# Kernel optimization log

Hardware: AMD Instinct MI355X
Metric: run time of the kernel (lower is better)

Reference implementation:

```python
import jax, jax.numpy as jnp
import numpy as np

B, S, D, N = 8, 4096, 1024, 64
EPS = 1e-5


def setup_inputs() -> dict:
    key = jax.random.key(0)
    ks = jax.random.split(key, 6)
    sD = 1.0 / np.sqrt(D)
    sN = 1.0 / np.sqrt(N)
    return {
        "x": jax.random.normal(ks[0], (B, S, D), dtype=jnp.float32),
        "ln_w": jnp.ones((D,), jnp.float32),
        "ln_b": jnp.zeros((D,), jnp.float32),
        "Wi": jax.random.normal(ks[1], (N, D), jnp.float32) * sD,
        "bi": jnp.zeros((N,), jnp.float32),
        "Wf": jax.random.normal(ks[2], (N, D), jnp.float32) * sD,
        "bf": jnp.zeros((N,), jnp.float32),
        "Wz": jax.random.normal(ks[3], (N, D), jnp.float32) * sD,
        "bz": jnp.zeros((N,), jnp.float32),
        "Wo": jax.random.normal(ks[4], (N, D), jnp.float32) * sD,
        "bo": jnp.zeros((N,), jnp.float32),
        "Wp": jax.random.normal(ks[5], (D, N), jnp.float32) * sN,
        "bp": jnp.zeros((D,), jnp.float32),
    }


def reference(x, ln_w, ln_b, Wi, bi, Wf, bf, Wz, bz, Wo, bo, Wp, bp):
    # LayerNorm over last dim (eps matches torch default 1e-5)
    mu = jnp.mean(x, axis=-1, keepdims=True)
    var = jnp.mean(jnp.square(x - mu), axis=-1, keepdims=True)
    xn = (x - mu) * jax.lax.rsqrt(var + EPS) * ln_w + ln_b

    # Precompute all four projections as batched GEMMs: (B,S,N)
    log_i = jnp.clip(jnp.einsum('bsd,nd->bsn', xn, Wi) + bi, -20.0, 20.0)
    log_f = jnp.clip(jnp.einsum('bsd,nd->bsn', xn, Wf) + bf, -20.0, 20.0)
    z = jnp.tanh(jnp.einsum('bsd,nd->bsn', xn, Wz) + bz)
    o = jax.nn.sigmoid(jnp.einsum('bsd,nd->bsn', xn, Wo) + bo)

    # Stabilized exponential-gated recurrence via lax.scan over time
    def step(carry, inp):
        c, m = carry
        li, lf, zt, ot = inp
        m_new = jnp.maximum(m + lf, li)
        i_s = jnp.exp(li - m_new)
        f_s = jnp.exp(m + lf - m_new)
        c = f_s * c + i_s * zt
        h = ot * jnp.tanh(c)
        return (c, m_new), h

    c0 = jnp.zeros((x.shape[0], log_i.shape[-1]), x.dtype)
    m0 = jnp.zeros_like(c0)
    # time-major inputs: (S,B,N)
    tm = lambda a: jnp.swapaxes(a, 0, 1)
    _, h_seq = jax.lax.scan(step, (c0, m0), (tm(log_i), tm(log_f), tm(z), tm(o)))
    h_seq = jnp.swapaxes(h_seq, 0, 1)  # (B,S,N)

    return jnp.einsum('bsn,dn->bsd', h_seq, Wp) + bp
```

## Files before the change

kernel.cpp:

```cpp
#include <hip/hip_runtime.h>
#include <hip/hip_bf16.h>

#define BB 8
#define SS 4096
#define DD 1024
#define NN 64
#define ROWS (BB * SS)
#define GLD 256
#define NCHUNK 256
#define CLEN 16

typedef _Float16 f16;
using f16x8 = __attribute__((ext_vector_type(8))) _Float16;
using f32x4 = __attribute__((ext_vector_type(4))) float;

__global__ void prep_pack(const float* __restrict__ Wi, const float* __restrict__ Wf,
                          const float* __restrict__ Wz, const float* __restrict__ Wo,
                          const float* __restrict__ Wp, const float* __restrict__ ln_w,
                          f16* __restrict__ Wpk, f16* __restrict__ Wpf) {
    int i = blockIdx.x * 256 + threadIdx.x;
    if (i < 32768) {
        int l = i & 63, cb = (i >> 6) & 15, s = i >> 10;
        int r = cb * 16 + (l & 15);
        int c = s * 32 + (l >> 4) * 8;
        int g = r >> 6, rem = r & 63;
        const float* W = (g == 0) ? Wi : (g == 1) ? Wf : (g == 2) ? Wz : Wo;
        const float* src = W + rem * 1024 + c;
        const float* lwp = ln_w + c;
        f16x8 v;
        #pragma unroll
        for (int e = 0; e < 8; ++e) v[e] = (f16)(src[e] * lwp[e]);
        *reinterpret_cast<f16x8*>(Wpk + (size_t)s * 8192 + cb * 512 + l * 8) = v;
    } else if (i < 32768 + 65536) {
        int j = i - 32768;
        Wpf[j] = (f16)Wp[j];
    }
}

__global__ __launch_bounds__(256) void prep_bias(const float* __restrict__ Wi, const float* __restrict__ bi,
                                                 const float* __restrict__ Wf, const float* __restrict__ bfv,
                                                 const float* __restrict__ Wz, const float* __restrict__ bz,
                                                 const float* __restrict__ Wo, const float* __restrict__ bo,
                                                 const float* __restrict__ ln_w, const float* __restrict__ ln_b,
                                                 float* __restrict__ ball, float* __restrict__ e_all) {
    int j = blockIdx.x * 4 + (threadIdx.x >> 6);
    int lane = threadIdx.x & 63;
    int g = j >> 6, rem = j & 63;
    const float* W  = (g == 0) ? Wi : (g == 1) ? Wf : (g == 2) ? Wz : Wo;
    const float* bs = (g == 0) ? bi : (g == 1) ? bfv : (g == 2) ? bz : bo;
    const float* row = W + rem * 1024;
    float d = 0.0f, e = 0.0f;
    #pragma unroll
    for (int t = 0; t < 16; ++t) {
        int k = lane + 64 * t;
        float w = row[k];
        e += ln_w[k] * w;
        d += ln_b[k] * w;
    }
    #pragma unroll
    for (int off = 1; off < 64; off <<= 1) {
        e += __shfl_xor(e, off);
        d += __shfl_xor(d, off);
    }
    if (lane == 0) { ball[j] = bs[rem] + d; e_all[j] = e; }
}

__global__ __launch_bounds__(512, 1) void gate_gemm(const float* __restrict__ x,
                                                    const f16* __restrict__ Wpk,
                                                    const float* __restrict__ ball,
                                                    const float* __restrict__ e_all,
                                                    float* __restrict__ gates) {
    int bm = blockIdx.x * 128;
    int tid = threadIdx.x;
    int wid = tid >> 6, lane = tid & 63;
    int wm = wid >> 2, wn = wid & 3;
    int lrow = lane & 15, lkg = lane >> 4;
    int srow = tid >> 2, skg = tid & 3;

    __shared__ __align__(16) f16 Wlds[2][16384];
    __shared__ __align__(16) f16 Xlds[2][8192];
    __shared__ float2 stats_lds[128];

    const float4* xrow = reinterpret_cast<const float4*>(x + (size_t)(bm + srow) * DD) + skg * 4;
    float4 A0, A1, A2, A3, B0, B1, B2, B3;
    uint4 W0, W1, W2, W3;
    const uint4* wsrc = reinterpret_cast<const uint4*>(Wpk) + wid * 256 + lane;

    auto loadA = [&](int s) { const float4* p = xrow + s * 16; A0 = p[0]; A1 = p[1]; A2 = p[2]; A3 = p[3]; };
    auto loadB = [&](int s) { const float4* p = xrow + s * 16; B0 = p[0]; B1 = p[1]; B2 = p[2]; B3 = p[3]; };
    auto loadW = [&](int s) { const uint4* p = wsrc + (size_t)s * 2048; W0 = p[0]; W1 = p[64]; W2 = p[128]; W3 = p[192]; };
    auto writeW = [&](int buf) {
        uint4* d = reinterpret_cast<uint4*>((char*)&Wlds[buf][0] + wid * 4096) + lane;
        d[0] = W0; d[64] = W1; d[128] = W2; d[192] = W3;
    };

    float s1 = 0.0f, s2 = 0.0f;
    auto writeXv = [&](float4 v0, float4 v1, float4 v2, float4 v3, int buf) {
        float xv[16] = {v0.x, v0.y, v0.z, v0.w, v1.x, v1.y, v1.z, v1.w,
                        v2.x, v2.y, v2.z, v2.w, v3.x, v3.y, v3.z, v3.w};
        f16x8 p0, p1;
        #pragma unroll
        for (int e = 0; e < 8; ++e) {
            s1 += xv[e] + xv[8 + e];
            s2 += xv[e] * xv[e] + xv[8 + e] * xv[8 + e];
            p0[e] = (f16)xv[e];
            p1[e] = (f16)xv[8 + e];
        }
        char* base = (char*)&Xlds[buf][0] + srow * 128;
        int r7 = srow & 7;
        *reinterpret_cast<f16x8*>(base + 16 * ((2 * skg) ^ r7))     = p0;
        *reinterpret_cast<f16x8*>(base + 16 * ((2 * skg + 1) ^ r7)) = p1;
    };

    f32x4 acc[4][4] = {};
    auto compute = [&](int buf) {
        #pragma unroll
        for (int h = 0; h < 2; ++h) {
            f16x8 a[4];
            #pragma unroll
            for (int mf = 0; mf < 4; ++mf) {
                int row = wm * 64 + mf * 16 + lrow;
                a[mf] = *reinterpret_cast<const f16x8*>(
                    (const char*)&Xlds[buf][0] + row * 128 + 16 * ((4 * h + lkg) ^ (row & 7)));
            }
            #pragma unroll
            for (int nf = 0; nf < 4; ++nf) {
                int cb = wn * 4 + nf;
                f16x8 w = *reinterpret_cast<const f16x8*>(
                    (const char*)&Wlds[buf][0] + h * 16384 + cb * 1024 + lane * 16);
                #pragma unroll
                for (int mf = 0; mf < 4; ++mf)
                    acc[mf][nf] = __builtin_amdgcn_mfma_f32_16x16x32_f16(a[mf], w, acc[mf][nf], 0, 0, 0);
            }
        }
    };
    auto stepSync = [&]() {
        asm volatile("s_waitcnt lgkmcnt(0)" ::: "memory");
        __builtin_amdgcn_s_barrier();
        __builtin_amdgcn_sched_barrier(0);
    };

    loadA(0); loadB(1); loadW(0);
    writeW(0);
    writeXv(A0, A1, A2, A3, 0);
    loadA(2); loadW(1);
    stepSync();

    for (int it = 0; it < 8; ++it) {
        int s = 2 * it;
        compute(0);
        writeW(1);
        writeXv(B0, B1, B2, B3, 1);
        if (s + 2 <= 15) loadW(s + 2);
        if (s + 3 <= 15) loadB(s + 3);
        stepSync();
        compute(1);
        if (s + 2 <= 15) {
            writeW(0);
            writeXv(A0, A1, A2, A3, 0);
        }
        if (s + 3 <= 15) loadW(s + 3);
        if (s + 4 <= 15) loadA(s + 4);
        stepSync();
    }

    s1 += __shfl_xor(s1, 1); s2 += __shfl_xor(s2, 1);
    s1 += __shfl_xor(s1, 2); s2 += __shfl_xor(s2, 2);
    if ((tid & 3) == 0) {
        float mu = s1 * (1.0f / DD);
        float var = s2 * (1.0f / DD) - mu * mu;
        float rsd = rsqrtf(var + 1e-5f);
        float2 st; st.x = mu * rsd; st.y = rsd;
        stats_lds[srow] = st;
    }
    __syncthreads();

    int c0 = wn * 64;
    int rb = (lane >> 4) * 4;
    #pragma unroll
    for (int mf = 0; mf < 4; ++mf) {
        #pragma unroll
        for (int nf = 0; nf < 4; ++nf) {
            int col = c0 + nf * 16 + (lane & 15);
            float bc = ball[col];
            float ec = e_all[col];
            #pragma unroll
            for (int r = 0; r < 4; ++r) {
                int rl = wm * 64 + mf * 16 + rb + r;
                float2 st = stats_lds[rl];
                float v = acc[mf][nf][r] * st.y + bc - st.x * ec;
                float res;
                if (wn == 0 || wn == 1)      res = fminf(fmaxf(v, -20.0f), 20.0f);
                else if (wn == 2)            res = tanhf(v);
                else                         res = 1.0f / (1.0f + expf(-v));
                gates[(size_t)(bm + rl) * GLD + col] = res;
            }
        }
    }
}

__global__ __launch_bounds__(256) void scan_a(const float* __restrict__ gates,
                                              float4* __restrict__ s4) {
    int w = blockIdx.x * 4 + (threadIdx.x >> 6);
    int lane = threadIdx.x & 63;
    int b = w >> 8, k = w & (NCHUNK - 1);
    int t0 = k * CLEN;
    const float* gp = gates + ((size_t)(b * SS + t0)) * GLD + lane;
    float Lf = 0.0f, m = -1e30f, c = 0.0f;
    for (int t = 0; t < CLEN; ++t) {
        float li = gp[0], lf = gp[64], z = gp[128];
        gp += GLD;
        Lf += lf;
        float ma = m + lf;
        float mn = fmaxf(ma, li);
        c = expf(ma - mn) * c + expf(li - mn) * z;
        m = mn;
    }
    float4 v; v.x = Lf; v.y = m; v.z = c; v.w = 0.0f;
    s4[(size_t)(b * NCHUNK + k) * 64 + lane] = v;
}

__global__ __launch_bounds__(64) void scan_b(const float4* __restrict__ s4,
                                             float2* __restrict__ c2) {
    int b = blockIdx.x;
    int n = threadIdx.x;
    size_t base = (size_t)b * NCHUNK * 64 + n;
    float c = 0.0f, m = 0.0f;
    float4 cur[16];
    #pragma unroll
    for (int d = 0; d < 16; ++d) cur[d] = s4[base + (size_t)d * 64];
    for (int kb = 0; kb < NCHUNK; kb += 16) {
        float4 nxt[16];
        if (kb + 16 < NCHUNK) {
            #pragma unroll
            for (int d = 0; d < 16; ++d) nxt[d] = s4[base + (size_t)(kb + 16 + d) * 64];
        }
        #pragma unroll
        for (int d = 0; d < 16; ++d) {
            float2 ci; ci.x = m; ci.y = c;
            c2[base + (size_t)(kb + d) * 64] = ci;
            float4 v = cur[d];
            float ma = m + v.x;
            float mo = fmaxf(ma, v.y);
            c = expf(ma - mo) * c + expf(v.y - mo) * v.z;
            m = mo;
        }
        #pragma unroll
        for (int d = 0; d < 16; ++d) cur[d] = nxt[d];
    }
}

__global__ __launch_bounds__(256) void scan_c(const float* __restrict__ gates,
                                              const float2* __restrict__ c2,
                                              f16* __restrict__ h) {
    int w = blockIdx.x * 4 + (threadIdx.x >> 6);
    int lane = threadIdx.x & 63;
    int b = w >> 8, k = w & (NCHUNK - 1);
    int t0 = k * CLEN;
    float2 ci = c2[(size_t)(b * NCHUNK + k) * 64 + lane];
    float m = ci.x, c = ci.y;
    const float* gp = gates + ((size_t)(b * SS + t0)) * GLD + lane;
    f16* hp = h + ((size_t)(b * SS + t0)) * NN + lane;
    for (int t = 0; t < CLEN; ++t) {
        float li = gp[0], lf = gp[64], z = gp[128], o = gp[192];
        gp += GLD;
        float ma = m + lf;
        float mn = fmaxf(ma, li);
        c = expf(ma - mn) * c + expf(li - mn) * z;
        m = mn;
        *hp = (f16)(o * tanhf(c));
        hp += NN;
    }
}

__global__ __launch_bounds__(256) void out_gemm(const f16* __restrict__ h,
                                                const f16* __restrict__ Wpf,
                                                const float* __restrict__ bp,
                                                float* __restrict__ out) {
    int tid = threadIdx.x, wid = tid >> 6, lane = tid & 63;
    int r0 = (blockIdx.x >> 1) * 32;
    int c0 = (blockIdx.x & 1) * 512 + wid * 128;
    int lrow = lane & 15, lk = (lane >> 4) * 8;

    f32x4 acc[2][8] = {};
    #pragma unroll
    for (int ks = 0; ks < 2; ++ks) {
        int kk = ks * 32;
        f16x8 a[2], bfr[8];
        #pragma unroll
        for (int mf = 0; mf < 2; ++mf)
            a[mf] = *reinterpret_cast<const f16x8*>(h + (size_t)(r0 + mf * 16 + lrow) * NN + kk + lk);
        #pragma unroll
        for (int nf = 0; nf < 8; ++nf)
            bfr[nf] = *reinterpret_cast<const f16x8*>(Wpf + (size_t)(c0 + nf * 16 + lrow) * NN + kk + lk);
        #pragma unroll
        for (int mf = 0; mf < 2; ++mf)
            #pragma unroll
            for (int nf = 0; nf < 8; ++nf)
                acc[mf][nf] = __builtin_amdgcn_mfma_f32_16x16x32_f16(a[mf], bfr[nf], acc[mf][nf], 0, 0, 0);
    }
    int rb = (lane >> 4) * 4;
    #pragma unroll
    for (int nf = 0; nf < 8; ++nf) {
        int col = c0 + nf * 16 + (lane & 15);
        float bias = bp[col];
        #pragma unroll
        for (int mf = 0; mf < 2; ++mf) {
            #pragma unroll
            for (int r = 0; r < 4; ++r) {
                int row = r0 + mf * 16 + rb + r;
                out[(size_t)row * DD + col] = acc[mf][nf][r] + bias;
            }
        }
    }
}

extern "C" void kernel_launch(void* const* d_in, const int* in_sizes, int n_in,
                              void* d_out, int out_size, void* d_ws, size_t ws_size,
                              hipStream_t stream) {
    const float* x    = (const float*)d_in[0];
    const float* ln_w = (const float*)d_in[1];
    const float* ln_b = (const float*)d_in[2];
    const float* Wi   = (const float*)d_in[3];
    const float* bi   = (const float*)d_in[4];
    const float* Wf   = (const float*)d_in[5];
    const float* bfv  = (const float*)d_in[6];
    const float* Wz   = (const float*)d_in[7];
    const float* bz   = (const float*)d_in[8];
    const float* Wo   = (const float*)d_in[9];
    const float* bo   = (const float*)d_in[10];
    const float* Wp   = (const float*)d_in[11];
    const float* bp   = (const float*)d_in[12];
    float* out = (float*)d_out;

    float* gates = (float*)d_out;
    float4* s4 = (float4*)((float*)d_out + 9 * 1024 * 1024);
    float2* c2 = (float2*)((float*)d_out + 10 * 1024 * 1024);

    char* w = (char*)d_ws;
    f16* h    = (f16*)w; w += (size_t)ROWS * NN * 2;
    f16* Wpk  = (f16*)w; w += 32 * 8192 * 2;
    f16* Wpf  = (f16*)w; w += 1024 * 64 * 2;
    float* ball   = (float*)w;    w += 256 * 4;
    float* e_all  = (float*)w;    w += 256 * 4;

    prep_pack<<<384, 256, 0, stream>>>(Wi, Wf, Wz, Wo, Wp, ln_w, Wpk, Wpf);
    prep_bias<<<64, 256, 0, stream>>>(Wi, bi, Wf, bfv, Wz, bz, Wo, bo, ln_w, ln_b, ball, e_all);
    gate_gemm<<<ROWS / 128, 512, 0, stream>>>(x, Wpk, ball, e_all, gates);
    scan_a<<<(BB * NCHUNK) / 4, 256, 0, stream>>>(gates, s4);
    scan_b<<<BB, 64, 0, stream>>>(s4, c2);
    scan_c<<<(BB * NCHUNK) / 4, 256, 0, stream>>>(gates, c2, h);
    out_gemm<<<(ROWS / 32) * 2, 256, 0, stream>>>(h, Wpf, bp, out);
}
```

Measured before the change: 132.9 us.

## Retile gate GEMM to 64-row blocks with K=32 steps and higher occupancy

The gate GEMM now uses 64-row tiles with 256 threads (4 waves, each covering 64 output columns) instead of 128-row tiles with 512 threads. The K step shrinks from 64 to 32, which changes the LDS layout, swizzle, load mapping and double-buffer pipeline, and launch bounds now target 3 blocks per CU. The aim is more resident blocks and twice as many blocks to hide global-load latency. The cost is twice as many weight tile reloads per row and more barriers per unit of work.

```diff
diff --git a/kernel.cpp b/kernel.cpp
--- a/kernel.cpp
+++ b/kernel.cpp
@@ -12,6 +12,7 @@
 
 typedef _Float16 f16;
 using f16x8 = __attribute__((ext_vector_type(8))) _Float16;
+using f16x4 = __attribute__((ext_vector_type(4))) _Float16;
 using f32x4 = __attribute__((ext_vector_type(4))) float;
 
 __global__ void prep_pack(const float* __restrict__ Wi, const float* __restrict__ Wf,
@@ -65,73 +66,71 @@
     if (lane == 0) { ball[j] = bs[rem] + d; e_all[j] = e; }
 }
 
-__global__ __launch_bounds__(512, 1) void gate_gemm(const float* __restrict__ x,
+__global__ __launch_bounds__(256, 3) void gate_gemm(const float* __restrict__ x,
                                                     const f16* __restrict__ Wpk,
                                                     const float* __restrict__ ball,
                                                     const float* __restrict__ e_all,
                                                     float* __restrict__ gates) {
-    int bm = blockIdx.x * 128;
+    int bm = blockIdx.x * 64;
     int tid = threadIdx.x;
-    int wid = tid >> 6, lane = tid & 63;
-    int wm = wid >> 2, wn = wid & 3;
+    int wn = tid >> 6, lane = tid & 63;
     int lrow = lane & 15, lkg = lane >> 4;
-    int srow = tid >> 2, skg = tid & 3;
-
-    __shared__ __align__(16) f16 Wlds[2][16384];
-    __shared__ __align__(16) f16 Xlds[2][8192];
-    __shared__ float2 stats_lds[128];
-
-    const float4* xrow = reinterpret_cast<const float4*>(x + (size_t)(bm + srow) * DD) + skg * 4;
-    float4 A0, A1, A2, A3, B0, B1, B2, B3;
-    uint4 W0, W1, W2, W3;
-    const uint4* wsrc = reinterpret_cast<const uint4*>(Wpk) + wid * 256 + lane;
-
-    auto loadA = [&](int s) { const float4* p = xrow + s * 16; A0 = p[0]; A1 = p[1]; A2 = p[2]; A3 = p[3]; };
-    auto loadB = [&](int s) { const float4* p = xrow + s * 16; B0 = p[0]; B1 = p[1]; B2 = p[2]; B3 = p[3]; };
-    auto loadW = [&](int s) { const uint4* p = wsrc + (size_t)s * 2048; W0 = p[0]; W1 = p[64]; W2 = p[128]; W3 = p[192]; };
-    auto writeW = [&](int buf) {
-        uint4* d = reinterpret_cast<uint4*>((char*)&Wlds[buf][0] + wid * 4096) + lane;
-        d[0] = W0; d[64] = W1; d[128] = W2; d[192] = W3;
-    };
-
-    float s1 = 0.0f, s2 = 0.0f;
-    auto writeXv = [&](float4 v0, float4 v1, float4 v2, float4 v3, int buf) {
-        float xv[16] = {v0.x, v0.y, v0.z, v0.w, v1.x, v1.y, v1.z, v1.w,
-                        v2.x, v2.y, v2.z, v2.w, v3.x, v3.y, v3.z, v3.w};
-        f16x8 p0, p1;
-        #pragma unroll
-        for (int e = 0; e < 8; ++e) {
-            s1 += xv[e] + xv[8 + e];
-            s2 += xv[e] * xv[e] + xv[8 + e] * xv[8 + e];
-            p0[e] = (f16)xv[e];
-            p1[e] = (f16)xv[8 + e];
-        }
-        char* base = (char*)&Xlds[buf][0] + srow * 128;
-        int r7 = srow & 7;
-        *reinterpret_cast<f16x8*>(base + 16 * ((2 * skg) ^ r7))     = p0;
-        *reinterpret_cast<f16x8*>(base + 16 * ((2 * skg + 1) ^ r7)) = p1;
+
+    __shared__ __align__(16) char Wlds[2][16384];
+    __shared__ __align__(16) char Xlds[2][4096];
+    __shared__ float2 stats_lds[64];
+
+    int xr0 = tid >> 3;
+    int xc4 = tid & 7;
+    const float4* xsrc = reinterpret_cast<const float4*>(x) + (size_t)(bm + xr0) * 256 + xc4;
+    const uint4* wsrc = reinterpret_cast<const uint4*>(Wpk) + tid;
+
+    float4 XA0, XA1, XB0, XB1;
+    uint4 WA0, WA1, WA2, WA3, WB0, WB1, WB2, WB3;
+
+    auto loadXA = [&](int s) { XA0 = xsrc[s * 8]; XA1 = xsrc[s * 8 + 32 * 256]; };
+    auto loadXB = [&](int s) { XB0 = xsrc[s * 8]; XB1 = xsrc[s * 8 + 32 * 256]; };
+    auto loadWA = [&](int s) { const uint4* p = wsrc + (size_t)s * 1024; WA0 = p[0]; WA1 = p[256]; WA2 = p[512]; WA3 = p[768]; };
+    auto loadWB = [&](int s) { const uint4* p = wsrc + (size_t)s * 1024; WB0 = p[0]; WB1 = p[256]; WB2 = p[512]; WB3 = p[768]; };
+
+    float sa1 = 0.0f, sa2 = 0.0f, sb1 = 0.0f, sb2 = 0.0f;
+    int xsl = (((xc4 >> 1) ^ (xr0 & 3)) << 4) + (xc4 & 1) * 8;
+    auto writeXv = [&](int buf, float4 v0, float4 v1) {
+        sa1 += v0.x + v0.y + v0.z + v0.w;
+        sa2 += v0.x * v0.x + v0.y * v0.y + v0.z * v0.z + v0.w * v0.w;
+        sb1 += v1.x + v1.y + v1.z + v1.w;
+        sb2 += v1.x * v1.x + v1.y * v1.y + v1.z * v1.z + v1.w * v1.w;
+        f16x4 p0, p1;
+        p0[0] = (f16)v0.x; p0[1] = (f16)v0.y; p0[2] = (f16)v0.z; p0[3] = (f16)v0.w;
+        p1[0] = (f16)v1.x; p1[1] = (f16)v1.y; p1[2] = (f16)v1.z; p1[3] = (f16)v1.w;
+        char* b = &Xlds[buf][0];
+        *reinterpret_cast<f16x4*>(b + xr0 * 64 + xsl) = p0;
+        *reinterpret_cast<f16x4*>(b + (xr0 + 32) * 64 + xsl) = p1;
+    };
+    auto writeWA = [&](int buf) {
+        uint4* d = reinterpret_cast<uint4*>(&Wlds[buf][0]) + tid;
+        d[0] = WA0; d[256] = WA1; d[512] = WA2; d[768] = WA3;
+    };
+    auto writeWB = [&](int buf) {
+        uint4* d = reinterpret_cast<uint4*>(&Wlds[buf][0]) + tid;
+        d[0] = WB0; d[256] = WB1; d[512] = WB2; d[768] = WB3;
     };
 
     f32x4 acc[4][4] = {};
     auto compute = [&](int buf) {
-        #pragma unroll
-        for (int h = 0; h < 2; ++h) {
-            f16x8 a[4];
-            #pragma unroll
-            for (int mf = 0; mf < 4; ++mf) {
-                int row = wm * 64 + mf * 16 + lrow;
-                a[mf] = *reinterpret_cast<const f16x8*>(
-                    (const char*)&Xlds[buf][0] + row * 128 + 16 * ((4 * h + lkg) ^ (row & 7)));
-            }
-            #pragma unroll
-            for (int nf = 0; nf < 4; ++nf) {
-                int cb = wn * 4 + nf;
-                f16x8 w = *reinterpret_cast<const f16x8*>(
-                    (const char*)&Wlds[buf][0] + h * 16384 + cb * 1024 + lane * 16);
-                #pragma unroll
-                for (int mf = 0; mf < 4; ++mf)
-                    acc[mf][nf] = __builtin_amdgcn_mfma_f32_16x16x32_f16(a[mf], w, acc[mf][nf], 0, 0, 0);
-            }
+        f16x8 a[4];
+        #pragma unroll
+        for (int mf = 0; mf < 4; ++mf) {
+            int row = mf * 16 + lrow;
+            a[mf] = *reinterpret_cast<const f16x8*>(&Xlds[buf][0] + row * 64 + ((lkg ^ (row & 3)) << 4));
+        }
+        #pragma unroll
+        for (int nf = 0; nf < 4; ++nf) {
+            int cb = wn * 4 + nf;
+            f16x8 w = *reinterpret_cast<const f16x8*>(&Wlds[buf][0] + cb * 1024 + lane * 16);
+            #pragma unroll
+            for (int mf = 0; mf < 4; ++mf)
+                acc[mf][nf] = __builtin_amdgcn_mfma_f32_16x16x32_f16(a[mf], w, acc[mf][nf], 0, 0, 0);
         }
     };
     auto stepSync = [&]() {
@@ -140,38 +139,41 @@
         __builtin_amdgcn_sched_barrier(0);
     };
 
-    loadA(0); loadB(1); loadW(0);
-    writeW(0);
-    writeXv(A0, A1, A2, A3, 0);
-    loadA(2); loadW(1);
+    loadXA(0); loadWA(0);
+    loadXB(1); loadWB(1);
+    writeWA(0); writeXv(0, XA0, XA1);
+    loadXA(2); loadWA(2);
     stepSync();
 
-    for (int it = 0; it < 8; ++it) {
+    for (int it = 0; it < 16; ++it) {
         int s = 2 * it;
         compute(0);
-        writeW(1);
-        writeXv(B0, B1, B2, B3, 1);
-        if (s + 2 <= 15) loadW(s + 2);
-        if (s + 3 <= 15) loadB(s + 3);
+        writeWB(1); writeXv(1, XB0, XB1);
+        if (s + 3 < 32) { loadXB(s + 3); loadWB(s + 3); }
         stepSync();
         compute(1);
-        if (s + 2 <= 15) {
-            writeW(0);
-            writeXv(A0, A1, A2, A3, 0);
-        }
-        if (s + 3 <= 15) loadW(s + 3);
-        if (s + 4 <= 15) loadA(s + 4);
+        if (s + 2 < 32) { writeWA(0); writeXv(0, XA0, XA1); }
+        if (s + 4 < 32) { loadXA(s + 4); loadWA(s + 4); }
         stepSync();
     }
 
-    s1 += __shfl_xor(s1, 1); s2 += __shfl_xor(s2, 1);
-    s1 += __shfl_xor(s1, 2); s2 += __shfl_xor(s2, 2);
-    if ((tid & 3) == 0) {
-        float mu = s1 * (1.0f / DD);
-        float var = s2 * (1.0f / DD) - mu * mu;
+    sa1 += __shfl_xor(sa1, 1); sa2 += __shfl_xor(sa2, 1);
+    sb1 += __shfl_xor(sb1, 1); sb2 += __shfl_xor(sb2, 1);
+    sa1 += __shfl_xor(sa1, 2); sa2 += __shfl_xor(sa2, 2);
+    sb1 += __shfl_xor(sb1, 2); sb2 += __shfl_xor(sb2, 2);
+    sa1 += __shfl_xor(sa1, 4); sa2 += __shfl_xor(sa2, 4);
+    sb1 += __shfl_xor(sb1, 4); sb2 += __shfl_xor(sb2, 4);
+    if ((tid & 7) == 0) {
+        float mu = sa1 * (1.0f / DD);
+        float var = sa2 * (1.0f / DD) - mu * mu;
         float rsd = rsqrtf(var + 1e-5f);
         float2 st; st.x = mu * rsd; st.y = rsd;
-        stats_lds[srow] = st;
+        stats_lds[xr0] = st;
+        mu = sb1 * (1.0f / DD);
+        var = sb2 * (1.0f / DD) - mu * mu;
+        rsd = rsqrtf(var + 1e-5f);
+        st.x = mu * rsd; st.y = rsd;
+        stats_lds[xr0 + 32] = st;
     }
     __syncthreads();
 
@@ -186,7 +188,7 @@
             float ec = e_all[col];
             #pragma unroll
             for (int r = 0; r < 4; ++r) {
-                int rl = wm * 64 + mf * 16 + rb + r;
+                int rl = mf * 16 + rb + r;
                 float2 st = stats_lds[rl];
                 float v = acc[mf][nf][r] * st.y + bc - st.x * ec;
                 float res;
@@ -346,7 +348,7 @@
 
     prep_pack<<<384, 256, 0, stream>>>(Wi, Wf, Wz, Wo, Wp, ln_w, Wpk, Wpf);
     prep_bias<<<64, 256, 0, stream>>>(Wi, bi, Wf, bfv, Wz, bz, Wo, bo, ln_w, ln_b, ball, e_all);
-    gate_gemm<<<ROWS / 128, 512, 0, stream>>>(x, Wpk, ball, e_all, gates);
+    gate_gemm<<<ROWS / 64, 256, 0, stream>>>(x, Wpk, ball, e_all, gates);
     scan_a<<<(BB * NCHUNK) / 4, 256, 0, stream>>>(gates, s4);
     scan_b<<<BB, 64, 0, stream>>>(s4, c2);
     scan_c<<<(BB * NCHUNK) / 4, 256, 0, stream>>>(gates, c2, h);
```

Result: slower. 179.7 us (+35.3%).

## Fuse chunk-summary scan into gate GEMM epilogue and merge prep kernels

Applied to the files above, without the earlier changes.

Merges the two weight-prep kernels into one launch, and moves the first scan pass (per-chunk summaries of log-forget sum, max and cell state) into the gate GEMM epilogue. The GEMM stages its gate results in reused LDS, and each wave scans one 16-step chunk, so scan_a no longer rereads the gates array from global memory. The cost is extra syncthreads, serialized epilogue phases with half the waves idle at a time, recomputation of activations for the second row half, and fast __expf in place of expf.

```diff
diff --git a/kernel.cpp b/kernel.cpp
--- a/kernel.cpp
+++ b/kernel.cpp
@@ -9,67 +9,68 @@
 #define GLD 256
 #define NCHUNK 256
 #define CLEN 16
+#define GSTRIDE 194
 
 typedef _Float16 f16;
 using f16x8 = __attribute__((ext_vector_type(8))) _Float16;
 using f32x4 = __attribute__((ext_vector_type(4))) float;
 
-__global__ void prep_pack(const float* __restrict__ Wi, const float* __restrict__ Wf,
-                          const float* __restrict__ Wz, const float* __restrict__ Wo,
-                          const float* __restrict__ Wp, const float* __restrict__ ln_w,
-                          f16* __restrict__ Wpk, f16* __restrict__ Wpf) {
-    int i = blockIdx.x * 256 + threadIdx.x;
-    if (i < 32768) {
-        int l = i & 63, cb = (i >> 6) & 15, s = i >> 10;
-        int r = cb * 16 + (l & 15);
-        int c = s * 32 + (l >> 4) * 8;
-        int g = r >> 6, rem = r & 63;
-        const float* W = (g == 0) ? Wi : (g == 1) ? Wf : (g == 2) ? Wz : Wo;
-        const float* src = W + rem * 1024 + c;
-        const float* lwp = ln_w + c;
-        f16x8 v;
-        #pragma unroll
-        for (int e = 0; e < 8; ++e) v[e] = (f16)(src[e] * lwp[e]);
-        *reinterpret_cast<f16x8*>(Wpk + (size_t)s * 8192 + cb * 512 + l * 8) = v;
-    } else if (i < 32768 + 65536) {
-        int j = i - 32768;
-        Wpf[j] = (f16)Wp[j];
-    }
-}
-
-__global__ __launch_bounds__(256) void prep_bias(const float* __restrict__ Wi, const float* __restrict__ bi,
-                                                 const float* __restrict__ Wf, const float* __restrict__ bfv,
-                                                 const float* __restrict__ Wz, const float* __restrict__ bz,
-                                                 const float* __restrict__ Wo, const float* __restrict__ bo,
-                                                 const float* __restrict__ ln_w, const float* __restrict__ ln_b,
-                                                 float* __restrict__ ball, float* __restrict__ e_all) {
-    int j = blockIdx.x * 4 + (threadIdx.x >> 6);
-    int lane = threadIdx.x & 63;
-    int g = j >> 6, rem = j & 63;
-    const float* W  = (g == 0) ? Wi : (g == 1) ? Wf : (g == 2) ? Wz : Wo;
-    const float* bs = (g == 0) ? bi : (g == 1) ? bfv : (g == 2) ? bz : bo;
-    const float* row = W + rem * 1024;
-    float d = 0.0f, e = 0.0f;
-    #pragma unroll
-    for (int t = 0; t < 16; ++t) {
-        int k = lane + 64 * t;
-        float w = row[k];
-        e += ln_w[k] * w;
-        d += ln_b[k] * w;
-    }
-    #pragma unroll
-    for (int off = 1; off < 64; off <<= 1) {
-        e += __shfl_xor(e, off);
-        d += __shfl_xor(d, off);
-    }
-    if (lane == 0) { ball[j] = bs[rem] + d; e_all[j] = e; }
+__global__ __launch_bounds__(256) void prep_all(const float* __restrict__ Wi, const float* __restrict__ bi,
+                                                const float* __restrict__ Wf, const float* __restrict__ bfv,
+                                                const float* __restrict__ Wz, const float* __restrict__ bz,
+                                                const float* __restrict__ Wo, const float* __restrict__ bo,
+                                                const float* __restrict__ Wp,
+                                                const float* __restrict__ ln_w, const float* __restrict__ ln_b,
+                                                f16* __restrict__ Wpk, f16* __restrict__ Wpf,
+                                                float* __restrict__ ball, float* __restrict__ e_all) {
+    if (blockIdx.x < 384) {
+        int i = blockIdx.x * 256 + threadIdx.x;
+        if (i < 32768) {
+            int l = i & 63, cb = (i >> 6) & 15, s = i >> 10;
+            int r = cb * 16 + (l & 15);
+            int c = s * 32 + (l >> 4) * 8;
+            int g = r >> 6, rem = r & 63;
+            const float* W = (g == 0) ? Wi : (g == 1) ? Wf : (g == 2) ? Wz : Wo;
+            const float* src = W + rem * 1024 + c;
+            const float* lwp = ln_w + c;
+            f16x8 v;
+            #pragma unroll
+            for (int e = 0; e < 8; ++e) v[e] = (f16)(src[e] * lwp[e]);
+            *reinterpret_cast<f16x8*>(Wpk + (size_t)s * 8192 + cb * 512 + l * 8) = v;
+        } else if (i < 32768 + 65536) {
+            int j = i - 32768;
+            Wpf[j] = (f16)Wp[j];
+        }
+    } else {
+        int j = (blockIdx.x - 384) * 4 + (threadIdx.x >> 6);
+        int lane = threadIdx.x & 63;
+        int g = j >> 6, rem = j & 63;
+        const float* W  = (g == 0) ? Wi : (g == 1) ? Wf : (g == 2) ? Wz : Wo;
+        const float* bs = (g == 0) ? bi : (g == 1) ? bfv : (g == 2) ? bz : bo;
+        const float* row = W + rem * 1024;
+        float d = 0.0f, e = 0.0f;
+        #pragma unroll
+        for (int t = 0; t < 16; ++t) {
+            int k = lane + 64 * t;
+            float w = row[k];
+            e += ln_w[k] * w;
+            d += ln_b[k] * w;
+        }
+        #pragma unroll
+        for (int off = 1; off < 64; off <<= 1) {
+            e += __shfl_xor(e, off);
+            d += __shfl_xor(d, off);
+        }
+        if (lane == 0) { ball[j] = bs[rem] + d; e_all[j] = e; }
+    }
 }
 
 __global__ __launch_bounds__(512, 1) void gate_gemm(const float* __restrict__ x,
                                                     const f16* __restrict__ Wpk,
                                                     const float* __restrict__ ball,
                                                     const float* __restrict__ e_all,
-                                                    float* __restrict__ gates) {
+                                                    float* __restrict__ gates,
+                                                    float4* __restrict__ s4) {
     int bm = blockIdx.x * 128;
     int tid = threadIdx.x;
     int wid = tid >> 6, lane = tid & 63;
@@ -175,6 +176,7 @@
     }
     __syncthreads();
 
+    float* glds = reinterpret_cast<float*>(&Wlds[0][0]);
     int c0 = wn * 64;
     int rb = (lane >> 4) * 4;
     #pragma unroll
@@ -194,30 +196,58 @@
                 else if (wn == 2)            res = tanhf(v);
                 else                         res = 1.0f / (1.0f + expf(-v));
                 gates[(size_t)(bm + rl) * GLD + col] = res;
-            }
-        }
-    }
-}
-
-__global__ __launch_bounds__(256) void scan_a(const float* __restrict__ gates,
-                                              float4* __restrict__ s4) {
-    int w = blockIdx.x * 4 + (threadIdx.x >> 6);
-    int lane = threadIdx.x & 63;
-    int b = w >> 8, k = w & (NCHUNK - 1);
-    int t0 = k * CLEN;
-    const float* gp = gates + ((size_t)(b * SS + t0)) * GLD + lane;
-    float Lf = 0.0f, m = -1e30f, c = 0.0f;
-    for (int t = 0; t < CLEN; ++t) {
-        float li = gp[0], lf = gp[64], z = gp[128];
-        gp += GLD;
-        Lf += lf;
-        float ma = m + lf;
-        float mn = fmaxf(ma, li);
-        c = expf(ma - mn) * c + expf(li - mn) * z;
-        m = mn;
-    }
-    float4 v; v.x = Lf; v.y = m; v.z = c; v.w = 0.0f;
-    s4[(size_t)(b * NCHUNK + k) * 64 + lane] = v;
+                if (wm == 0 && wn < 3)
+                    glds[(mf * 16 + rb + r) * GSTRIDE + col] = res;
+            }
+        }
+    }
+    __syncthreads();
+
+    int b = bm >> 12;
+    int cb0 = (bm & 4095) >> 4;
+    auto scanChunk = [&]() {
+        int lr0 = (wid & 3) * 16;
+        float Lf = 0.0f, m = -1e30f, c = 0.0f;
+        #pragma unroll
+        for (int j = 0; j < 16; ++j) {
+            const float* g = glds + (lr0 + j) * GSTRIDE;
+            float li = g[lane], lf = g[64 + lane], z = g[128 + lane];
+            Lf += lf;
+            float ma = m + lf;
+            float mn = fmaxf(ma, li);
+            c = __expf(ma - mn) * c + __expf(li - mn) * z;
+            m = mn;
+        }
+        float4 v; v.x = Lf; v.y = m; v.z = c; v.w = 0.0f;
+        s4[(size_t)(b * NCHUNK + cb0 + wid) * 64 + lane] = v;
+    };
+
+    if (wm == 0) scanChunk();
+    __syncthreads();
+
+    if (wm == 1 && wn < 3) {
+        #pragma unroll
+        for (int mf = 0; mf < 4; ++mf) {
+            #pragma unroll
+            for (int nf = 0; nf < 4; ++nf) {
+                int col = c0 + nf * 16 + (lane & 15);
+                float bc = ball[col];
+                float ec = e_all[col];
+                #pragma unroll
+                for (int r = 0; r < 4; ++r) {
+                    int rl = 64 + mf * 16 + rb + r;
+                    float2 st = stats_lds[rl];
+                    float v = acc[mf][nf][r] * st.y + bc - st.x * ec;
+                    float res;
+                    if (wn == 0 || wn == 1)      res = fminf(fmaxf(v, -20.0f), 20.0f);
+                    else                         res = tanhf(v);
+                    glds[(mf * 16 + rb + r) * GSTRIDE + col] = res;
+                }
+            }
+        }
+    }
+    __syncthreads();
+    if (wm == 1) scanChunk();
 }
 
 __global__ __launch_bounds__(64) void scan_b(const float4* __restrict__ s4,
@@ -344,10 +374,9 @@
     float* ball   = (float*)w;    w += 256 * 4;
     float* e_all  = (float*)w;    w += 256 * 4;
 
-    prep_pack<<<384, 256, 0, stream>>>(Wi, Wf, Wz, Wo, Wp, ln_w, Wpk, Wpf);
-    prep_bias<<<64, 256, 0, stream>>>(Wi, bi, Wf, bfv, Wz, bz, Wo, bo, ln_w, ln_b, ball, e_all);
-    gate_gemm<<<ROWS / 128, 512, 0, stream>>>(x, Wpk, ball, e_all, gates);
-    scan_a<<<(BB * NCHUNK) / 4, 256, 0, stream>>>(gates, s4);
+    prep_all<<<448, 256, 0, stream>>>(Wi, bi, Wf, bfv, Wz, bz, Wo, bo, Wp,
+                                      ln_w, ln_b, Wpk, Wpf, ball, e_all);
+    gate_gemm<<<ROWS / 128, 512, 0, stream>>>(x, Wpk, ball, e_all, gates, s4);
     scan_b<<<BB, 64, 0, stream>>>(s4, c2);
     scan_c<<<(BB * NCHUNK) / 4, 256, 0, stream>>>(gates, c2, h);
     out_gemm<<<(ROWS / 32) * 2, 256, 0, stream>>>(h, Wpf, bp, out);
```

New measurement: 135.9 us. 2.3% more time.
